# Optimization experiments

Measured on AMD Instinct MI355X. Metric: run time of the kernel, lower is better.

The kernel has to match this reference:

```python
import math
import jax, jax.numpy as jnp
import numpy as np

B, T, D = 2048, 50, 256
NEG = -100000.0

def setup_inputs() -> dict:
    key = jax.random.key(0)
    ks = jax.random.split(key, 9)
    return {
        "x": jax.random.normal(ks[0], (B, T, D), dtype=jnp.float32),
        "mask": jax.random.randint(ks[1], (B, T, 1), 0, 2, dtype=jnp.int32),
        "time_decay": jax.random.uniform(ks[2], (B, T, 1), dtype=jnp.float32),
        "Wq": jax.random.normal(ks[3], (D, D), dtype=jnp.float32) * (1.0 / math.sqrt(D)),
        "bq": jax.random.normal(ks[4], (D,), dtype=jnp.float32) * 0.01,
        "Wk": jax.random.normal(ks[5], (D, D), dtype=jnp.float32) * (1.0 / math.sqrt(D)),
        "bk": jax.random.normal(ks[6], (D,), dtype=jnp.float32) * 0.01,
        "Wv": jax.random.normal(ks[7], (D, D), dtype=jnp.float32) * (1.0 / math.sqrt(D)),
        "bv": jax.random.normal(ks[8], (D,), dtype=jnp.float32) * 0.01,
    }

def reference(x, mask, time_decay, Wq, bq, Wk, bk, Wv, bv):
    # PositionalEncoding.forward: elementwise multiply by time-decay (broadcast over d_model)
    x = x * time_decay  # [B,T,D]
    q = jnp.einsum('btd,ed->bte', x, Wq) + bq
    k = jnp.einsum('btd,ed->bte', x, Wk) + bk
    v = jnp.einsum('btd,ed->bte', x, Wv) + bv
    # unusual Q/K-side masking (masked_fill before the matmul)
    keep = mask != 0  # [B,T,1]
    q = jnp.where(keep, q, NEG)
    k = jnp.where(keep, k, NEG)
    score = jnp.einsum('btd,bsd->bts', q, k) / math.sqrt(D)  # [B,T,T]
    score = jax.nn.softmax(score, axis=-1)
    # dropout is identity in eval mode
    out = jnp.einsum('bts,bsd->btd', score, v)  # [B,T,D]
    return out[:, -1, :]  # [B,D]
```

## Files before the change

### kernel.cpp

```cpp
#include <hip/hip_runtime.h>


namespace {
constexpr int kB = 2048;
constexpr int kT = 50;
constexpr int kD = 256;
constexpr double kNeg = -100000.0;
constexpr int oM2 = 0;
constexpr int oWvp = 65536;
constexpr int oV0 = 131072;
constexpr int oC = 131328;
constexpr int oW1 = 131584;
constexpr int oW2 = 131840;
constexpr int oDbl = 132096;
}

__global__ __launch_bounds__(256) void precomp(
    const float* __restrict__ Wq, const float* __restrict__ bq,
    const float* __restrict__ Wk, const float* __restrict__ bk,
    const float* __restrict__ Wv, float* __restrict__ ws) {
  const int t = threadIdx.x;
  const int wave = t >> 6;
  const int lane = t & 63;
  const int blk = blockIdx.x;
  __shared__ float coefL[kD];
  __shared__ double red[3][4];

  if (blk < 256) {
    const int a = blk;
    coefL[t] = Wq[(size_t)t * kD + a];
    __syncthreads();
    const float* kcol = Wk + t;
    float pre[8];
#pragma unroll
    for (int k = 0; k < 8; ++k) pre[k] = kcol[(size_t)k * kD];
    float acc = 0.f;
    for (int j0 = 0; j0 < kD; j0 += 8) {
      float cur[8];
#pragma unroll
      for (int k = 0; k < 8; ++k) cur[k] = pre[k];
      const int nx = (j0 + 8 < kD) ? (j0 + 8) : 0;
#pragma unroll
      for (int k = 0; k < 8; ++k) pre[k] = kcol[(size_t)(nx + k) * kD];
#pragma unroll
      for (int k = 0; k < 8; ++k) acc += coefL[j0 + k] * cur[k];
    }
    ws[oM2 + (a >> 2) * 1024 + 4 * t + (a & 3)] = acc;
  } else if (blk < 258) {
    const float* W = (blk == 256) ? Wk : Wq;
    const float* coef = (blk == 256) ? bq : bk;
    coefL[t] = coef[t];
    __syncthreads();
    const float* col = W + t;
    float pre[8];
#pragma unroll
    for (int k = 0; k < 8; ++k) pre[k] = col[(size_t)k * kD];
    double a0 = 0.0, a1 = 0.0;
    for (int j0 = 0; j0 < kD; j0 += 8) {
      float cur[8];
#pragma unroll
      for (int k = 0; k < 8; ++k) cur[k] = pre[k];
      const int nx = (j0 + 8 < kD) ? (j0 + 8) : 0;
#pragma unroll
      for (int k = 0; k < 8; ++k) pre[k] = col[(size_t)(nx + k) * kD];
#pragma unroll
      for (int k = 0; k < 8; ++k) {
        const double w = (double)cur[k];
        a0 += (double)coefL[j0 + k] * w;
        a1 += w;
      }
    }
    if (blk == 256) {
      ws[oV0 + t] = (float)a0;
      ws[oC + t] = (float)a1;
    } else {
      ws[oW1 + t] = (float)a0;
      ws[oW2 + t] = (float)a1;
      double p0 = (double)bk[t];
      double p1 = (double)bq[t] * (double)bk[t];
      double p2 = (double)bq[t];
#pragma unroll
      for (int off = 32; off; off >>= 1) {
        p0 += __shfl_xor(p0, off);
        p1 += __shfl_xor(p1, off);
        p2 += __shfl_xor(p2, off);
      }
      if (lane == 0) {
        red[0][wave] = p0;
        red[1][wave] = p1;
        red[2][wave] = p2;
      }
      __syncthreads();
      if (t == 0) {
        double* dcw = (double*)(ws + oDbl);
        dcw[0] = red[0][0] + red[0][1] + red[0][2] + red[0][3];
        dcw[1] = red[1][0] + red[1][1] + red[1][2] + red[1][3];
        dcw[2] = red[2][0] + red[2][1] + red[2][2] + red[2][3];
      }
    }
  } else {
    const int d4b = (blk - 258) * 4;
    float4 in[4];
#pragma unroll
    for (int k = 0; k < 4; ++k)
      in[k] = *(const float4*)(Wv + (size_t)t * kD + 4 * (d4b + k));
    float4* Wvp = (float4*)(ws + oWvp);
#pragma unroll
    for (int k = 0; k < 4; ++k) Wvp[(size_t)(d4b + k) * kD + t] = in[k];
  }
}

__global__ __launch_bounds__(256) void fused_main(
    const float* __restrict__ x, const int* __restrict__ mask,
    const float* __restrict__ td, const float* __restrict__ bv,
    const float* __restrict__ ws, float* __restrict__ out) {
  const int tid = threadIdx.x;
  const int lane = tid & 63;
  const int w = tid >> 6;
  const int b0 = blockIdx.x * 2;
  __shared__ __align__(16) float xsL[2][kD];
  __shared__ __align__(16) float uL[2][kD];
  __shared__ __align__(16) float yL[2][kD];
  __shared__ __align__(16) float ypart[2][2][kD];
  __shared__ double mpart[2][2];
  __shared__ float lpart[2][2];
  __shared__ double dScal[2][2];

  const double* dc = (const double*)(ws + oDbl);
  const float4* M2v = (const float4*)(ws + oM2);
  const float4* Wvv = (const float4*)(ws + oWvp);

  const int ja = w >> 1;
  const int h = w & 1;
  const float mtdA = (lane < kT) ? td[(size_t)(b0 + ja) * kT + lane] : 0.f;
  const int mmkA = (lane < kT) ? mask[(size_t)(b0 + ja) * kT + lane] : 0;
  const float4 c4 = ((const float4*)(ws + oC))[lane];

  if (h == 0) {
    const int j = ja;
    const int b = b0 + j;
    const float tdl = __shfl(mtdA, kT - 1);
    const float4 a1 = ((const float4*)(ws + oW1))[lane];
    const float4 a2 = ((const float4*)(ws + oW2))[lane];
    const float4 xv =
        ((const float4*)(x + ((size_t)b * kT + kT - 1) * kD))[lane];
    double s1 = (double)xv.x * a1.x + (double)xv.y * a1.y +
                (double)xv.z * a1.z + (double)xv.w * a1.w;
    double s2 = (double)xv.x * a2.x + (double)xv.y * a2.y +
                (double)xv.z * a2.z + (double)xv.w * a2.w;
#pragma unroll
    for (int off = 32; off; off >>= 1) {
      s1 += __shfl_xor(s1, off);
      s2 += __shfl_xor(s2, off);
    }
    if (lane == 0) {
      dScal[j][0] = (double)tdl * s1 + dc[1];
      dScal[j][1] = (double)tdl * s2 + dc[2];
    }
    float4 xs;
    xs.x = xv.x * tdl; xs.y = xv.y * tdl;
    xs.z = xv.z * tdl; xs.w = xv.w * tdl;
    *(float4*)(&xsL[j][4 * lane]) = xs;
  }
  __syncthreads();

  {
    const int col = 64 * w + lane;
    float4 A = M2v[col];
    float4 B = M2v[256 + col];
    float acc0 = 0.f, acc1 = 0.f;
    for (int k4 = 0; k4 < 64; k4 += 2) {
      const float4 c0 = A, c1 = B;
      const int n0 = (k4 + 2 < 64) ? k4 + 2 : 0;
      const int n1 = (k4 + 3 < 64) ? k4 + 3 : 1;
      A = M2v[(size_t)n0 * 256 + col];
      B = M2v[(size_t)n1 * 256 + col];
      const float4 x00 = *(const float4*)(&xsL[0][4 * k4]);
      const float4 x01 = *(const float4*)(&xsL[0][4 * (k4 + 1)]);
      const float4 x10 = *(const float4*)(&xsL[1][4 * k4]);
      const float4 x11 = *(const float4*)(&xsL[1][4 * (k4 + 1)]);
      acc0 += x00.x * c0.x + x00.y * c0.y + x00.z * c0.z + x00.w * c0.w +
              x01.x * c1.x + x01.y * c1.y + x01.z * c1.z + x01.w * c1.w;
      acc1 += x10.x * c0.x + x10.y * c0.y + x10.z * c0.z + x10.w * c0.w +
              x11.x * c1.x + x11.y * c1.y + x11.z * c1.z + x11.w * c1.w;
    }
    const float v0g = ws[oV0 + col];
    uL[0][col] = acc0 + v0g;
    uL[1][col] = acc1 + v0g;
  }
  __syncthreads();

  {
    const int j = ja;
    const int b = b0 + j;
    const float mtd = mtdA;
    const int mmk = mmkA;
    const int mqg = __shfl(mmk, kT - 1);
    const float4 u4 = *(const float4*)(&uL[j][4 * lane]);
    const float4 v4 = mqg ? u4 : c4;
    const double Qb = dScal[j][0];
    const double Cm = kNeg * dScal[j][1] * 0.0625;
    const double sbkd = dc[0];
    const double Cbb = 256.0 * 1.0e10 * 0.0625;
    const int sbeg = h ? 24 : 0;
    const int slim = h ? 52 : 24;

    const float4* xrow = (const float4*)(x + (size_t)b * kT * kD);
    double m = -1.0e300;
    float l = 0.f;
    float4 y = {0.f, 0.f, 0.f, 0.f};

    float4 n0 = xrow[(size_t)(sbeg + 0) * 64 + lane];
    float4 n1 = xrow[(size_t)(sbeg + 1) * 64 + lane];
    float4 n2 = xrow[(size_t)(sbeg + 2) * 64 + lane];
    float4 n3 = xrow[(size_t)(sbeg + 3) * 64 + lane];
    for (int s = sbeg; s < slim; s += 4) {
      const float4 r0 = n0, r1 = n1, r2 = n2, r3 = n3;
      {
        const int p0 = (s + 4 < kT) ? s + 4 : kT - 1;
        const int p1 = (s + 5 < kT) ? s + 5 : kT - 1;
        const int p2 = (s + 6 < kT) ? s + 6 : kT - 1;
        const int p3 = (s + 7 < kT) ? s + 7 : kT - 1;
        n0 = xrow[(size_t)p0 * 64 + lane];
        n1 = xrow[(size_t)p1 * 64 + lane];
        n2 = xrow[(size_t)p2 * 64 + lane];
        n3 = xrow[(size_t)p3 * 64 + lane];
      }
      const int s1i = s + 1, s2i = s + 2, s3i = s + 3;
      const int cc0 = s;
      const int cc1 = (s1i < kT) ? s1i : kT - 1;
      const int cc2 = (s2i < kT) ? s2i : kT - 1;
      const int cc3 = (s3i < kT) ? s3i : kT - 1;
      const float tv0 = __shfl(mtd, cc0);
      const float tv1 = __shfl(mtd, cc1);
      const float tv2 = __shfl(mtd, cc2);
      const float tv3 = __shfl(mtd, cc3);
      float4 a0, aa1, a2v, a3;
      a0.x = r0.x * tv0; a0.y = r0.y * tv0; a0.z = r0.z * tv0; a0.w = r0.w * tv0;
      aa1.x = r1.x * tv1; aa1.y = r1.y * tv1; aa1.z = r1.z * tv1; aa1.w = r1.w * tv1;
      a2v.x = r2.x * tv2; a2v.y = r2.y * tv2; a2v.z = r2.z * tv2; a2v.w = r2.w * tv2;
      a3.x = r3.x * tv3; a3.y = r3.y * tv3; a3.z = r3.z * tv3; a3.w = r3.w * tv3;
      float p0 = a0.x * v4.x + a0.y * v4.y + a0.z * v4.z + a0.w * v4.w;
      float p1 = aa1.x * v4.x + aa1.y * v4.y + aa1.z * v4.z + aa1.w * v4.w;
      float p2 = a2v.x * v4.x + a2v.y * v4.y + a2v.z * v4.z + a2v.w * v4.w;
      float p3 = a3.x * v4.x + a3.y * v4.y + a3.z * v4.z + a3.w * v4.w;
#pragma unroll
      for (int off = 32; off; off >>= 1) {
        p0 += __shfl_xor(p0, off);
        p1 += __shfl_xor(p1, off);
        p2 += __shfl_xor(p2, off);
        p3 += __shfl_xor(p3, off);
      }
      const int ms0 = __shfl(mmk, cc0);
      const int ms1 = __shfl(mmk, cc1);
      const int ms2 = __shfl(mmk, cc2);
      const int ms3 = __shfl(mmk, cc3);
      double sc0, sc1, sc2, sc3;
      if (mqg) {
        sc0 = ms0 ? ((double)p0 + Qb) * 0.0625 : Cm;
        sc1 = ms1 ? ((double)p1 + Qb) * 0.0625 : Cm;
        sc2 = ms2 ? ((double)p2 + Qb) * 0.0625 : Cm;
        sc3 = ms3 ? ((double)p3 + Qb) * 0.0625 : Cm;
      } else {
        sc0 = ms0 ? kNeg * ((double)p0 + sbkd) * 0.0625 : Cbb;
        sc1 = ms1 ? kNeg * ((double)p1 + sbkd) * 0.0625 : Cbb;
        sc2 = ms2 ? kNeg * ((double)p2 + sbkd) * 0.0625 : Cbb;
        sc3 = ms3 ? kNeg * ((double)p3 + sbkd) * 0.0625 : Cbb;
      }
      if (s1i >= kT) sc1 = -1.0e300;
      if (s2i >= kT) sc2 = -1.0e300;
      if (s3i >= kT) sc3 = -1.0e300;
      double mnew = m;
      if (sc0 > mnew) mnew = sc0;
      if (sc1 > mnew) mnew = sc1;
      if (sc2 > mnew) mnew = sc2;
      if (sc3 > mnew) mnew = sc3;
      const float al = expf((float)(m - mnew));
      const float e0 = expf((float)(sc0 - mnew));
      const float e1 = expf((float)(sc1 - mnew));
      const float e2 = expf((float)(sc2 - mnew));
      const float e3 = expf((float)(sc3 - mnew));
      m = mnew;
      l = l * al + e0 + e1 + e2 + e3;
      y.x = y.x * al + e0 * a0.x + e1 * aa1.x + e2 * a2v.x + e3 * a3.x;
      y.y = y.y * al + e0 * a0.y + e1 * aa1.y + e2 * a2v.y + e3 * a3.y;
      y.z = y.z * al + e0 * a0.z + e1 * aa1.z + e2 * a2v.z + e3 * a3.z;
      y.w = y.w * al + e0 * a0.w + e1 * aa1.w + e2 * a2v.w + e3 * a3.w;
    }
    if (lane == 0) {
      mpart[j][h] = m;
      lpart[j][h] = l;
    }
    *(float4*)(&ypart[j][h][4 * lane]) = y;
  }
  __syncthreads();

  if (h == 0) {
    const int j = ja;
    const double m0 = mpart[j][0], m1 = mpart[j][1];
    const double M = (m0 > m1) ? m0 : m1;
    const float e0 = expf((float)(m0 - M));
    const float e1 = expf((float)(m1 - M));
    const float l = lpart[j][0] * e0 + lpart[j][1] * e1;
    const float inv = 1.0f / l;
    const float4 y0 = *(const float4*)(&ypart[j][0][4 * lane]);
    const float4 y1 = *(const float4*)(&ypart[j][1][4 * lane]);
    float4 yv;
    yv.x = (y0.x * e0 + y1.x * e1) * inv;
    yv.y = (y0.y * e0 + y1.y * e1) * inv;
    yv.z = (y0.z * e0 + y1.z * e1) * inv;
    yv.w = (y0.w * e0 + y1.w * e1) * inv;
    *(float4*)(&yL[j][4 * lane]) = yv;
  }
  __syncthreads();

  {
    const int col = 64 * w + lane;
    float4 A = Wvv[col];
    float4 B = Wvv[256 + col];
    float acc0 = 0.f, acc1 = 0.f;
    for (int k4 = 0; k4 < 64; k4 += 2) {
      const float4 c0 = A, c1 = B;
      const int n0 = (k4 + 2 < 64) ? k4 + 2 : 0;
      const int n1 = (k4 + 3 < 64) ? k4 + 3 : 1;
      A = Wvv[(size_t)n0 * 256 + col];
      B = Wvv[(size_t)n1 * 256 + col];
      const float4 y00 = *(const float4*)(&yL[0][4 * k4]);
      const float4 y01 = *(const float4*)(&yL[0][4 * (k4 + 1)]);
      const float4 y10 = *(const float4*)(&yL[1][4 * k4]);
      const float4 y11 = *(const float4*)(&yL[1][4 * (k4 + 1)]);
      acc0 += y00.x * c0.x + y00.y * c0.y + y00.z * c0.z + y00.w * c0.w +
              y01.x * c1.x + y01.y * c1.y + y01.z * c1.z + y01.w * c1.w;
      acc1 += y10.x * c0.x + y10.y * c0.y + y10.z * c0.z + y10.w * c0.w +
              y11.x * c1.x + y11.y * c1.y + y11.z * c1.z + y11.w * c1.w;
    }
    const float bvg = bv[col];
    out[(size_t)(b0 + 0) * kD + col] = acc0 + bvg;
    out[(size_t)(b0 + 1) * kD + col] = acc1 + bvg;
  }
}

extern "C" void kernel_launch(void* const* d_in, const int* in_sizes, int n_in,
                              void* d_out, int out_size, void* d_ws,
                              size_t ws_size, hipStream_t stream) {
  const float* x = (const float*)d_in[0];
  const int* mask = (const int*)d_in[1];
  const float* td = (const float*)d_in[2];
  const float* Wq = (const float*)d_in[3];
  const float* bq = (const float*)d_in[4];
  const float* Wk = (const float*)d_in[5];
  const float* bk = (const float*)d_in[6];
  const float* Wv = (const float*)d_in[7];
  const float* bv = (const float*)d_in[8];
  float* ws = (float*)d_ws;
  float* out = (float*)d_out;
  (void)in_sizes; (void)n_in; (void)out_size; (void)ws_size;

  hipLaunchKernelGGL(precomp, dim3(274), dim3(256), 0, stream, Wq, bq, Wk, bk,
                     Wv, ws);
  hipLaunchKernelGGL(fused_main, dim3(kB / 2), dim3(256), 0, stream, x, mask,
                     td, bv, (const float*)ws, out);
}
```

Measured before the change: 197.6 us.

## Double block to 512 threads, split attention and GEMVs across more waves

Raises fused_main to 512 threads (8 waves) per two-batch block. Each batch's 50 key positions are now split over four waves instead of two, and both 256x256 GEMVs are split along K into two halves reduced through shared memory. The softmax merge now runs on all threads. Exp calls become __expf. The aim is more parallelism per block to hide memory latency, at the cost of extra barriers, shared-memory reductions and lower-precision exp.

```diff
diff --git a/kernel.cpp b/kernel.cpp
--- a/kernel.cpp
+++ b/kernel.cpp
@@ -110,7 +110,7 @@
   }
 }
 
-__global__ __launch_bounds__(256) void fused_main(
+__global__ __launch_bounds__(512, 8) void fused_main(
     const float* __restrict__ x, const int* __restrict__ mask,
     const float* __restrict__ td, const float* __restrict__ bv,
     const float* __restrict__ ws, float* __restrict__ out) {
@@ -121,22 +121,22 @@
   __shared__ __align__(16) float xsL[2][kD];
   __shared__ __align__(16) float uL[2][kD];
   __shared__ __align__(16) float yL[2][kD];
-  __shared__ __align__(16) float ypart[2][2][kD];
-  __shared__ double mpart[2][2];
-  __shared__ float lpart[2][2];
+  __shared__ __align__(16) float scr[2][4][kD];
+  __shared__ double mpart[2][4];
+  __shared__ float lpart[2][4];
   __shared__ double dScal[2][2];
 
   const double* dc = (const double*)(ws + oDbl);
   const float4* M2v = (const float4*)(ws + oM2);
   const float4* Wvv = (const float4*)(ws + oWvp);
 
-  const int ja = w >> 1;
-  const int h = w & 1;
+  const int ja = w >> 2;
+  const int q = w & 3;
   const float mtdA = (lane < kT) ? td[(size_t)(b0 + ja) * kT + lane] : 0.f;
   const int mmkA = (lane < kT) ? mask[(size_t)(b0 + ja) * kT + lane] : 0;
   const float4 c4 = ((const float4*)(ws + oC))[lane];
 
-  if (h == 0) {
+  if (q == 0) {
     const int j = ja;
     const int b = b0 + j;
     const float tdl = __shfl(mtdA, kT - 1);
@@ -165,14 +165,17 @@
   __syncthreads();
 
   {
-    const int col = 64 * w + lane;
-    float4 A = M2v[col];
-    float4 B = M2v[256 + col];
+    const int gU = w >> 1;
+    const int kh = w & 1;
+    const int col = 64 * gU + lane;
+    const int kb = kh * 32;
+    float4 A = M2v[(size_t)kb * 256 + col];
+    float4 B = M2v[(size_t)(kb + 1) * 256 + col];
     float acc0 = 0.f, acc1 = 0.f;
-    for (int k4 = 0; k4 < 64; k4 += 2) {
+    for (int k4 = kb; k4 < kb + 32; k4 += 2) {
       const float4 c0 = A, c1 = B;
-      const int n0 = (k4 + 2 < 64) ? k4 + 2 : 0;
-      const int n1 = (k4 + 3 < 64) ? k4 + 3 : 1;
+      const int n0 = (k4 + 2 < kb + 32) ? k4 + 2 : kb;
+      const int n1 = (k4 + 3 < kb + 32) ? k4 + 3 : kb + 1;
       A = M2v[(size_t)n0 * 256 + col];
       B = M2v[(size_t)n1 * 256 + col];
       const float4 x00 = *(const float4*)(&xsL[0][4 * k4]);
@@ -184,9 +187,15 @@
       acc1 += x10.x * c0.x + x10.y * c0.y + x10.z * c0.z + x10.w * c0.w +
               x11.x * c1.x + x11.y * c1.y + x11.z * c1.z + x11.w * c1.w;
     }
-    const float v0g = ws[oV0 + col];
-    uL[0][col] = acc0 + v0g;
-    uL[1][col] = acc1 + v0g;
+    scr[kh][0][col] = acc0;
+    scr[kh][1][col] = acc1;
+  }
+  __syncthreads();
+
+  {
+    const int mj = tid >> 8;
+    const int mcol = tid & 255;
+    uL[mj][mcol] = scr[0][mj][mcol] + scr[1][mj][mcol] + ws[oV0 + mcol];
   }
   __syncthreads();
 
@@ -202,19 +211,23 @@
     const double Cm = kNeg * dScal[j][1] * 0.0625;
     const double sbkd = dc[0];
     const double Cbb = 256.0 * 1.0e10 * 0.0625;
-    const int sbeg = h ? 24 : 0;
-    const int slim = h ? 52 : 24;
+    const int sbeg = (q == 0) ? 0 : (q == 1) ? 13 : (q == 2) ? 26 : 38;
+    const int send = (q == 0) ? 13 : (q == 1) ? 26 : (q == 2) ? 38 : 50;
 
     const float4* xrow = (const float4*)(x + (size_t)b * kT * kD);
     double m = -1.0e300;
     float l = 0.f;
     float4 y = {0.f, 0.f, 0.f, 0.f};
 
-    float4 n0 = xrow[(size_t)(sbeg + 0) * 64 + lane];
-    float4 n1 = xrow[(size_t)(sbeg + 1) * 64 + lane];
-    float4 n2 = xrow[(size_t)(sbeg + 2) * 64 + lane];
-    float4 n3 = xrow[(size_t)(sbeg + 3) * 64 + lane];
-    for (int s = sbeg; s < slim; s += 4) {
+    const int i0 = (sbeg + 0 < kT) ? sbeg + 0 : kT - 1;
+    const int i1 = (sbeg + 1 < kT) ? sbeg + 1 : kT - 1;
+    const int i2 = (sbeg + 2 < kT) ? sbeg + 2 : kT - 1;
+    const int i3 = (sbeg + 3 < kT) ? sbeg + 3 : kT - 1;
+    float4 n0 = xrow[(size_t)i0 * 64 + lane];
+    float4 n1 = xrow[(size_t)i1 * 64 + lane];
+    float4 n2 = xrow[(size_t)i2 * 64 + lane];
+    float4 n3 = xrow[(size_t)i3 * 64 + lane];
+    for (int s = sbeg; s < send; s += 4) {
       const float4 r0 = n0, r1 = n1, r2 = n2, r3 = n3;
       {
         const int p0 = (s + 4 < kT) ? s + 4 : kT - 1;
@@ -267,19 +280,19 @@
         sc2 = ms2 ? kNeg * ((double)p2 + sbkd) * 0.0625 : Cbb;
         sc3 = ms3 ? kNeg * ((double)p3 + sbkd) * 0.0625 : Cbb;
       }
-      if (s1i >= kT) sc1 = -1.0e300;
-      if (s2i >= kT) sc2 = -1.0e300;
-      if (s3i >= kT) sc3 = -1.0e300;
+      if (s1i >= send) sc1 = -1.0e300;
+      if (s2i >= send) sc2 = -1.0e300;
+      if (s3i >= send) sc3 = -1.0e300;
       double mnew = m;
       if (sc0 > mnew) mnew = sc0;
       if (sc1 > mnew) mnew = sc1;
       if (sc2 > mnew) mnew = sc2;
       if (sc3 > mnew) mnew = sc3;
-      const float al = expf((float)(m - mnew));
-      const float e0 = expf((float)(sc0 - mnew));
-      const float e1 = expf((float)(sc1 - mnew));
-      const float e2 = expf((float)(sc2 - mnew));
-      const float e3 = expf((float)(sc3 - mnew));
+      const float al = __expf((float)(m - mnew));
+      const float e0 = __expf((float)(sc0 - mnew));
+      const float e1 = __expf((float)(sc1 - mnew));
+      const float e2 = __expf((float)(sc2 - mnew));
+      const float e3 = __expf((float)(sc3 - mnew));
       m = mnew;
       l = l * al + e0 + e1 + e2 + e3;
       y.x = y.x * al + e0 * a0.x + e1 * aa1.x + e2 * a2v.x + e3 * a3.x;
@@ -288,41 +301,47 @@
       y.w = y.w * al + e0 * a0.w + e1 * aa1.w + e2 * a2v.w + e3 * a3.w;
     }
     if (lane == 0) {
-      mpart[j][h] = m;
-      lpart[j][h] = l;
-    }
-    *(float4*)(&ypart[j][h][4 * lane]) = y;
-  }
-  __syncthreads();
-
-  if (h == 0) {
-    const int j = ja;
-    const double m0 = mpart[j][0], m1 = mpart[j][1];
-    const double M = (m0 > m1) ? m0 : m1;
-    const float e0 = expf((float)(m0 - M));
-    const float e1 = expf((float)(m1 - M));
-    const float l = lpart[j][0] * e0 + lpart[j][1] * e1;
+      mpart[j][q] = m;
+      lpart[j][q] = l;
+    }
+    *(float4*)(&scr[j][q][4 * lane]) = y;
+  }
+  __syncthreads();
+
+  {
+    const int mj = tid >> 8;
+    const int mcol = tid & 255;
+    double M = mpart[mj][0];
+    if (mpart[mj][1] > M) M = mpart[mj][1];
+    if (mpart[mj][2] > M) M = mpart[mj][2];
+    if (mpart[mj][3] > M) M = mpart[mj][3];
+    const float e0 = __expf((float)(mpart[mj][0] - M));
+    const float e1 = __expf((float)(mpart[mj][1] - M));
+    const float e2 = __expf((float)(mpart[mj][2] - M));
+    const float e3 = __expf((float)(mpart[mj][3] - M));
+    const float l = lpart[mj][0] * e0 + lpart[mj][1] * e1 +
+                    lpart[mj][2] * e2 + lpart[mj][3] * e3;
     const float inv = 1.0f / l;
-    const float4 y0 = *(const float4*)(&ypart[j][0][4 * lane]);
-    const float4 y1 = *(const float4*)(&ypart[j][1][4 * lane]);
-    float4 yv;
-    yv.x = (y0.x * e0 + y1.x * e1) * inv;
-    yv.y = (y0.y * e0 + y1.y * e1) * inv;
-    yv.z = (y0.z * e0 + y1.z * e1) * inv;
-    yv.w = (y0.w * e0 + y1.w * e1) * inv;
-    *(float4*)(&yL[j][4 * lane]) = yv;
-  }
-  __syncthreads();
-
-  {
-    const int col = 64 * w + lane;
-    float4 A = Wvv[col];
-    float4 B = Wvv[256 + col];
+    const float yv = (scr[mj][0][mcol] * e0 + scr[mj][1][mcol] * e1 +
+                      scr[mj][2][mcol] * e2 + scr[mj][3][mcol] * e3) *
+                     inv;
+    __syncthreads();
+    yL[mj][mcol] = yv;
+  }
+  __syncthreads();
+
+  {
+    const int gU = w >> 1;
+    const int kh = w & 1;
+    const int col = 64 * gU + lane;
+    const int kb = kh * 32;
+    float4 A = Wvv[(size_t)kb * 256 + col];
+    float4 B = Wvv[(size_t)(kb + 1) * 256 + col];
     float acc0 = 0.f, acc1 = 0.f;
-    for (int k4 = 0; k4 < 64; k4 += 2) {
+    for (int k4 = kb; k4 < kb + 32; k4 += 2) {
       const float4 c0 = A, c1 = B;
-      const int n0 = (k4 + 2 < 64) ? k4 + 2 : 0;
-      const int n1 = (k4 + 3 < 64) ? k4 + 3 : 1;
+      const int n0 = (k4 + 2 < kb + 32) ? k4 + 2 : kb;
+      const int n1 = (k4 + 3 < kb + 32) ? k4 + 3 : kb + 1;
       A = Wvv[(size_t)n0 * 256 + col];
       B = Wvv[(size_t)n1 * 256 + col];
       const float4 y00 = *(const float4*)(&yL[0][4 * k4]);
@@ -334,9 +353,16 @@
       acc1 += y10.x * c0.x + y10.y * c0.y + y10.z * c0.z + y10.w * c0.w +
               y11.x * c1.x + y11.y * c1.y + y11.z * c1.z + y11.w * c1.w;
     }
-    const float bvg = bv[col];
-    out[(size_t)(b0 + 0) * kD + col] = acc0 + bvg;
-    out[(size_t)(b0 + 1) * kD + col] = acc1 + bvg;
+    scr[kh][0][col] = acc0;
+    scr[kh][1][col] = acc1;
+  }
+  __syncthreads();
+
+  {
+    const int mj = tid >> 8;
+    const int mcol = tid & 255;
+    out[(size_t)(b0 + mj) * kD + mcol] =
+        scr[0][mj][mcol] + scr[1][mj][mcol] + bv[mcol];
   }
 }
 
@@ -358,6 +384,6 @@
 
   hipLaunchKernelGGL(precomp, dim3(274), dim3(256), 0, stream, Wq, bq, Wk, bk,
                      Wv, ws);
-  hipLaunchKernelGGL(fused_main, dim3(kB / 2), dim3(256), 0, stream, x, mask,
+  hipLaunchKernelGGL(fused_main, dim3(kB / 2), dim3(512), 0, stream, x, mask,
                      td, bv, (const float*)ws, out);
 }
```

Result: slower. 288.3 us (+45.9%).
